# Optimization experiments

Hardware: AMD Instinct MI355X
Metric: run time of the kernel (lower is better)

## Reference

```python
import jax, jax.numpy as jnp
import numpy as np

B, N, D, Q, H = 8, 2048, 64, 16, 2
C = 2 * D + 1          # combined dim = 129
C8 = C // 8            # per-head qk dim = 16
K = 8192               # number of observed nodes
NEG = -9.0e15


def setup_inputs() -> dict:
    key = jax.random.key(0)
    ks = jax.random.split(key, 18)
    s = 0.05
    inp = {
        "x": jax.random.normal(ks[0], (B, N, D + 1), jnp.float32),
        "h": jax.random.normal(ks[1], (B, N, D), jnp.float32),
        "query_vectors": jax.random.normal(ks[2], (K, Q), jnp.float32),
        "adj": jax.random.randint(ks[3], (B, N, N), 0, 2, jnp.int32),
        "nodes_flat": jnp.arange(K, dtype=jnp.int32),
        # per-head attention projections (jax convention: x @ W + b)
        "Wq": jax.random.normal(ks[4], (H, C, C8), jnp.float32) * s,
        "bq": jax.random.normal(ks[5], (H, C8), jnp.float32) * s,
        "Wk": jax.random.normal(ks[6], (H, C, C8), jnp.float32) * s,
        "bk": jax.random.normal(ks[7], (H, C8), jnp.float32) * s,
        "Wv": jax.random.normal(ks[8], (H, C, C), jnp.float32) * s,
        "bv": jax.random.normal(ks[9], (H, C), jnp.float32) * s,
        # hypernetwork MLP_Param weights for reset / update / candidate gates
        "W_r": jax.random.normal(ks[10], (Q, C, D), jnp.float32) * s,
        "b_r": jax.random.normal(ks[11], (Q, D), jnp.float32) * s,
        "W_u": jax.random.normal(ks[12], (Q, C, D), jnp.float32) * s,
        "b_u": jax.random.normal(ks[13], (Q, D), jnp.float32) * s,
        "W_c": jax.random.normal(ks[14], (Q, C, D), jnp.float32) * s,
        "b_c": jax.random.normal(ks[15], (Q, D), jnp.float32) * s,
    }
    return inp


def _gate(x_sel, qv, W, b):
    # MLP_Param: W_n = einsum('nd,dio->nio', qv, W); out = x @ W_n + qv @ b
    # contract the combined dim first to avoid the [K, C, D] intermediate
    t = jnp.einsum('kc,qco->kqo', x_sel, W)      # [K, Q, D]
    return jnp.einsum('kq,kqo->ko', qv, t) + qv @ b


def reference(x, h, query_vectors, adj, nodes_flat,
              Wq, bq, Wk, bk, Wv, bv,
              W_r, b_r, W_u, b_u, W_c, b_c):
    combined = jnp.concatenate([x, h], axis=-1)                 # [B, N, C]
    q = jnp.einsum('bnc,hcd->hbnd', combined, Wq) + bq[:, None, None, :]
    k = jnp.einsum('bnc,hcd->hbnd', combined, Wk) + bk[:, None, None, :]
    v = jnp.einsum('bnc,hcd->hbnd', combined, Wv) + bv[:, None, None, :]
    scores = jnp.einsum('hbnd,hbmd->hbnm', q, k) / jnp.sqrt(jnp.float32(C8))
    scores = jax.nn.leaky_relu(scores, 0.2)
    scores = jnp.where(adj[None] == 0, NEG, scores)
    attn = jax.nn.softmax(scores, axis=-1)                      # [H, B, N, N]
    h_prime = jnp.einsum('hbnm,hbmc->hbnc', attn, v)
    comb_attn = h_prime.mean(axis=0)                            # [B, N, C]

    sel = comb_attn.reshape(-1, C)[nodes_flat]                  # [K, C]
    r = jax.nn.sigmoid(_gate(sel, query_vectors, W_r, b_r))     # [K, D]
    u = jax.nn.sigmoid(_gate(sel, query_vectors, W_u, b_u))     # [K, D]

    h_flat = h.reshape(-1, D)
    h_sel = r * h_flat[nodes_flat]                              # r * h[nodes_ind]
    h_flat = h_flat.at[nodes_flat].set(h_sel)
    h_new = h_flat.reshape(h.shape)

    comb_new = jnp.concatenate([x, h_new], axis=-1)             # [B, N, C]
    sel2 = comb_new.reshape(-1, C)[nodes_flat]
    cand = jnp.tanh(_gate(sel2, query_vectors, W_c, b_c))       # [K, D]

    return (1.0 - u) * h_sel + u * cand                         # [K, D]
```

## Files before the change

### kernel.cpp

```cpp
#include <hip/hip_runtime.h>
#include <hip/hip_bf16.h>


typedef _Float16 h2_t __attribute__((ext_vector_type(2)));
typedef _Float16 h8_t __attribute__((ext_vector_type(8)));
typedef float    f4_t __attribute__((ext_vector_type(4)));
#define MFMA16x32(a,b,c) __builtin_amdgcn_mfma_f32_16x16x32_f16(a,b,c,0,0,0)

#define OB_QG    0
#define OB_KG    524288
#define OB_VT    1048576
#define OB_MASK  5767168
#define OB_WALL  7864320
#define OB_HACC  7971840
#define OB_LSUM  16622592
#define OB_UBUF  16688128
#define OB_HSEL  18785280

__global__ __launch_bounds__(256) void pack_adj(const int* __restrict__ adj,
                                                unsigned* __restrict__ mask) {
    long tg = (long)blockIdx.x * 256 + threadIdx.x;
    for (int it = 0; it < 32; ++it) {
        long i = tg + (long)it * 524288;
        int a = adj[i];
        unsigned long long bal = __ballot(a != 0);
        if ((threadIdx.x & 63) == 0)
            *(unsigned long long*)(mask + (i >> 5)) = bal;
    }
}

__global__ __launch_bounds__(256) void repack_wall(
    const float* __restrict__ Wq, const float* __restrict__ bq,
    const float* __restrict__ Wk, const float* __restrict__ bk,
    const float* __restrict__ Wv, const float* __restrict__ bv,
    _Float16* __restrict__ Wall) {
    int idx = blockIdx.x * 256 + threadIdx.x;
    if (idx >= 6720) return;
    int ct = idx / 320;
    int rem = idx % 320;
    int s = rem >> 6, lane = rem & 63;
    int n = ct * 16 + (lane & 15);
    int quad = lane >> 4;
    int h2 = (n >= 164) ? 1 : 0;
    int nn = n - h2 * 164;
    h8_t v;
    #pragma unroll
    for (int j = 0; j < 8; ++j) {
        int k = s * 32 + quad * 8 + j;
        float f = 0.f;
        if (n < 328) {
            if (nn < 16) {
                if (k < 129)       f = Wq[(h2 * 129 + k) * 16 + nn];
                else if (k == 129) f = bq[h2 * 16 + nn];
            } else if (nn < 32) {
                int d = nn - 16;
                if (k < 129)       f = Wk[(h2 * 129 + k) * 16 + d];
                else if (k == 129) f = bk[h2 * 16 + d];
            } else {
                int vc = nn - 32;
                if (vc < 129) {
                    if (k < 129)       f = Wv[(h2 * 129 + k) * 129 + vc];
                    else if (k == 129) f = bv[h2 * 129 + vc];
                }
            }
        }
        v[j] = (_Float16)f;
    }
    *(h8_t*)(Wall + (size_t)idx * 8) = v;
}

__global__ __launch_bounds__(256) void repack_gates(
    const float* __restrict__ Wr, const float* __restrict__ br,
    const float* __restrict__ Wu, const float* __restrict__ bu,
    const float* __restrict__ Wc, const float* __restrict__ bc,
    _Float16* __restrict__ WtRu, _Float16* __restrict__ WtC) {
    int idx = blockIdx.x * 256 + threadIdx.x;
    if (idx < 35328) {
        int s = idx / 512;
        int rem = idx % 512;
        int ct = rem >> 6, lane = rem & 63;
        int o = ct * 16 + (lane & 15);
        int quad = lane >> 4;
        const float* W = (o < 64) ? Wr : Wu;
        const float* bb = (o < 64) ? br : bu;
        int oc = o & 63;
        h8_t v;
        #pragma unroll
        for (int j = 0; j < 8; ++j) {
            int kk = s * 32 + quad * 8 + j;
            float f = 0.f;
            if (kk < 2176) {
                int q = kk / 136, c = kk % 136;
                if (c < 129) f = W[(q * 129 + c) * 64 + oc];
            } else if (kk < 2192) {
                f = bb[(kk - 2176) * 64 + oc];
            }
            v[j] = (_Float16)f;
        }
        *(h8_t*)(WtRu + (size_t)idx * 8) = v;
    } else if (idx < 52992) {
        int i2 = idx - 35328;
        int s = i2 / 256;
        int rem = i2 % 256;
        int ct = rem >> 6, lane = rem & 63;
        int o = ct * 16 + (lane & 15);
        int quad = lane >> 4;
        h8_t v;
        #pragma unroll
        for (int j = 0; j < 8; ++j) {
            int kk = s * 32 + quad * 8 + j;
            float f = 0.f;
            if (kk < 2176) {
                int q = kk / 136, c = kk % 136;
                if (c < 129) f = Wc[(q * 129 + c) * 64 + o];
            } else if (kk < 2192) {
                f = bc[(kk - 2176) * 64 + o];
            }
            v[j] = (_Float16)f;
        }
        *(h8_t*)(WtC + (size_t)i2 * 8) = v;
    }
}

__global__ __launch_bounds__(256) void qkv_mfma(
    const float* __restrict__ x, const float* __restrict__ h,
    const _Float16* __restrict__ Wall,
    _Float16* __restrict__ qg, _Float16* __restrict__ kg,
    _Float16* __restrict__ vT) {
    __shared__ _Float16 at[16 * 168];
    int t = threadIdx.x;
    int row0 = blockIdx.x * 16;
    for (int idx = t; idx < 16 * 160; idx += 256) {
        int r = idx / 160, c = idx % 160;
        int grow = row0 + r;
        float v = 0.f;
        if (c < 65)       v = x[grow * 65 + c];
        else if (c < 129) v = h[grow * 64 + (c - 65)];
        else if (c == 129) v = 1.0f;
        at[r * 168 + c] = (_Float16)v;
    }
    __syncthreads();
    int lane = t & 63, w = t >> 6;
    int l16 = lane & 15, quad = lane >> 4;
    for (int ct = w; ct < 21; ct += 4) {
        f4_t acc; acc[0]=0.f; acc[1]=0.f; acc[2]=0.f; acc[3]=0.f;
        int n = ct * 16 + l16;
        const _Float16* wp = Wall + ((size_t)ct * 320 + lane) * 8;
        #pragma unroll
        for (int s = 0; s < 5; ++s) {
            h8_t a = *(const h8_t*)(at + l16 * 168 + s * 32 + quad * 8);
            h8_t b = *(const h8_t*)(wp + (size_t)s * 512);
            acc = MFMA16x32(a, b, acc);
        }
        if (n < 328) {
            int h2 = (n >= 164) ? 1 : 0;
            int nn = n - h2 * 164;
            #pragma unroll
            for (int r = 0; r < 4; ++r) {
                int grow = row0 + quad * 4 + r;
                _Float16 v = (_Float16)acc[r];
                if (nn < 16)      qg[(h2 * 8192 + grow) * 16 + nn] = v;
                else if (nn < 32) kg[(h2 * 8192 + grow) * 16 + (nn - 16)] = v;
                else              vT[((size_t)(h2 * 144 + (nn - 32))) * 8192 + grow] = v;
            }
        }
    }
}

__global__ __launch_bounds__(256) void attn_fused(
    const _Float16* __restrict__ qg, const _Float16* __restrict__ kg,
    const _Float16* __restrict__ vT, const unsigned* __restrict__ mask,
    float* __restrict__ hacc, float* __restrict__ lsum, int tps) {
    __shared__ _Float16 vsm[144 * 88];
    __shared__ _Float16 pT[4 * 16 * 88];
    int t = threadIdx.x;
    int nt = blockIdx.x, hb = blockIdx.y, sp = blockIdx.z;
    int h2 = hb >> 2, b = hb & 3;
    int base = h2 * 8192 + b * 2048;
    int n0 = nt * 64;
    int lane = t & 63, w = t >> 6;
    int l16 = lane & 15, q = lane >> 4;
    int qrow = n0 + w * 16 + l16;
    _Float16* pTw = pT + w * 16 * 88;
    h8_t zero8;
    #pragma unroll
    for (int i = 0; i < 8; ++i) zero8[i] = (_Float16)0.f;
    h8_t qf = zero8;
    if (q < 2) qf = *(const h8_t*)(qg + (base + qrow) * 16 + 8 * q);
    const unsigned* mrw = mask + (b * 2048 + qrow) * 64;
    f4_t acc[9];
    #pragma unroll
    for (int i = 0; i < 9; ++i) { acc[i][0]=0.f; acc[i][1]=0.f; acc[i][2]=0.f; acc[i][3]=0.f; }
    float l_run = 0.f;
    for (int mt = sp * tps; mt < sp * tps + tps; ++mt) {
        int m0 = mt * 64;
        __syncthreads();
        for (int idx = t; idx < 1152; idx += 256) {
            int c = idx >> 3, ch = idx & 7;
            *(uint4*)(vsm + c * 88 + ch * 8) =
                *(const uint4*)(vT + ((size_t)h2 * 144 + c) * 8192 + b * 2048 + m0 + ch * 8);
        }
        __syncthreads();
        uint2 mw = *(const uint2*)(mrw + (m0 >> 5));
        f4_t st[4];
        #pragma unroll
        for (int ct = 0; ct < 4; ++ct) {
            h8_t kf = zero8;
            if (q < 2)
                kf = *(const h8_t*)(kg + (base + m0 + 16 * ct + l16) * 16 + 8 * q);
            f4_t z4; z4[0]=0.f; z4[1]=0.f; z4[2]=0.f; z4[3]=0.f;
            st[ct] = MFMA16x32(kf, qf, z4);
        }
        #pragma unroll
        for (int ct = 0; ct < 4; ++ct) {
            unsigned wb = (ct < 2) ? mw.x : mw.y;
            float p[4];
            #pragma unroll
            for (int r = 0; r < 4; ++r) {
                float sc = st[ct][r] * 0.25f;
                sc = sc > 0.f ? sc : 0.2f * sc;
                int bit = ((ct & 1) ? 16 : 0) + 4 * q + r;
                p[r] = ((wb >> bit) & 1u) ? __expf(sc) : 0.f;
                l_run += p[r];
            }
            h2_t p01; p01[0] = (_Float16)p[0]; p01[1] = (_Float16)p[1];
            h2_t p23; p23[0] = (_Float16)p[2]; p23[1] = (_Float16)p[3];
            *(h2_t*)(pTw + l16 * 88 + 16 * ct + 4 * q)     = p01;
            *(h2_t*)(pTw + l16 * 88 + 16 * ct + 4 * q + 2) = p23;
        }
        #pragma unroll
        for (int kh = 0; kh < 2; ++kh) {
            h8_t ap = *(const h8_t*)(pTw + l16 * 88 + 32 * kh + 8 * q);
            #pragma unroll
            for (int nb = 0; nb < 9; ++nb) {
                h8_t vf = *(const h8_t*)(vsm + (16 * nb + l16) * 88 + 32 * kh + 8 * q);
                acc[nb] = MFMA16x32(ap, vf, acc[nb]);
            }
        }
    }
    l_run += __shfl_xor(l_run, 16);
    l_run += __shfl_xor(l_run, 32);
    float* hc = hacc + (size_t)h2 * 8192 * 132;
    if (q == 0)
        atomicAdd(lsum + h2 * 8192 + b * 2048 + n0 + w * 16 + l16, l_run);
    #pragma unroll
    for (int nb = 0; nb < 9; ++nb) {
        int vc = 16 * nb + l16;
        if (vc < 132) {
            #pragma unroll
            for (int r = 0; r < 4; ++r) {
                int grow = b * 2048 + n0 + w * 16 + 4 * q + r;
                atomicAdd(hc + grow * 132 + vc, acc[nb][r]);
            }
        }
    }
}

__global__ __launch_bounds__(256) void gate_ru_mfma(
    const float* __restrict__ hacc, const float* __restrict__ lsum,
    const int* __restrict__ nodes,
    const float* __restrict__ qv, const _Float16* __restrict__ WtRu,
    const float* __restrict__ hbuf,
    float* __restrict__ ubuf, float* __restrict__ hsel) {
    __shared__ _Float16 selh[16 * 152];
    __shared__ float qvs[16 * 17];
    __shared__ float invl[32];
    int t = threadIdx.x;
    int k0 = blockIdx.x * 16;
    if (t < 32) {
        int r = t >> 1, hh = t & 1;
        int grow = nodes[k0 + r];
        invl[t] = 0.5f / lsum[hh * 8192 + grow];
    }
    __syncthreads();
    for (int idx = t; idx < 16 * 136; idx += 256) {
        int r = idx / 136, c = idx % 136;
        _Float16 v = (_Float16)0.f;
        if (c < 132) {
            int grow = nodes[k0 + r];
            v = (_Float16)(hacc[grow * 132 + c] * invl[r * 2] +
                           hacc[8192 * 132 + grow * 132 + c] * invl[r * 2 + 1]);
        }
        selh[r * 152 + c] = v;
    }
    if (t < 256) {
        int r = t >> 4, q = t & 15;
        qvs[r * 17 + q] = qv[(k0 + r) * 16 + q];
    }
    __syncthreads();
    int lane = t & 63, w = t >> 6;
    int l16 = lane & 15, quad = lane >> 4;
    f4_t acc0, acc1;
    acc0[0]=0.f;acc0[1]=0.f;acc0[2]=0.f;acc0[3]=0.f;
    acc1[0]=0.f;acc1[1]=0.f;acc1[2]=0.f;acc1[3]=0.f;
    const _Float16* wp0 = WtRu + ((size_t)(2 * w) * 64 + lane) * 8;
    const _Float16* wp1 = wp0 + 512;
    for (int step = 0; step < 69; ++step) {
        h8_t a;
        if (step < 68) {
            int chunk = 4 * step + quad;
            int q = chunk / 17;
            int c0 = (chunk - q * 17) * 8;
            h8_t s8 = *(const h8_t*)(selh + l16 * 152 + c0);
            _Float16 qh = (_Float16)qvs[l16 * 17 + q];
            #pragma unroll
            for (int j = 0; j < 8; ++j) a[j] = s8[j] * qh;
        } else {
            int kl = quad * 8;
            #pragma unroll
            for (int j = 0; j < 8; ++j) {
                int kq = kl + j;
                a[j] = (kq < 16) ? (_Float16)qvs[l16 * 17 + kq] : (_Float16)0.f;
            }
        }
        h8_t b0 = *(const h8_t*)(wp0 + (size_t)step * 4096);
        h8_t b1 = *(const h8_t*)(wp1 + (size_t)step * 4096);
        acc0 = MFMA16x32(a, b0, acc0);
        acc1 = MFMA16x32(a, b1, acc1);
    }
    #pragma unroll
    for (int tt = 0; tt < 2; ++tt) {
        f4_t ac = tt ? acc1 : acc0;
        int o = (2 * w + tt) * 16 + l16;
        #pragma unroll
        for (int r = 0; r < 4; ++r) {
            int k = k0 + quad * 4 + r;
            float sg = 1.f / (1.f + __expf(-ac[r]));
            if (o < 64) {
                int grow = nodes[k];
                hsel[k * 64 + o] = sg * hbuf[grow * 64 + o];
            } else {
                ubuf[k * 64 + (o - 64)] = sg;
            }
        }
    }
}

__global__ __launch_bounds__(256) void gate_c_mfma(
    const float* __restrict__ x, const int* __restrict__ nodes,
    const float* __restrict__ qv, const _Float16* __restrict__ WtC,
    const float* __restrict__ hsel, const float* __restrict__ ubuf,
    float* __restrict__ out) {
    __shared__ _Float16 selh[16 * 152];
    __shared__ float qvs[16 * 17];
    int t = threadIdx.x;
    int k0 = blockIdx.x * 16;
    for (int idx = t; idx < 16 * 136; idx += 256) {
        int r = idx / 136, c = idx % 136;
        int k = k0 + r;
        _Float16 v = (_Float16)0.f;
        if (c < 65) {
            int grow = nodes[k];
            v = (_Float16)x[grow * 65 + c];
        } else if (c < 129) {
            v = (_Float16)hsel[k * 64 + (c - 65)];
        }
        selh[r * 152 + c] = v;
    }
    if (t < 256) {
        int r = t >> 4, q = t & 15;
        qvs[r * 17 + q] = qv[(k0 + r) * 16 + q];
    }
    __syncthreads();
    int lane = t & 63, w = t >> 6;
    int l16 = lane & 15, quad = lane >> 4;
    f4_t acc;
    acc[0]=0.f;acc[1]=0.f;acc[2]=0.f;acc[3]=0.f;
    const _Float16* wp = WtC + ((size_t)w * 64 + lane) * 8;
    for (int step = 0; step < 69; ++step) {
        h8_t a;
        if (step < 68) {
            int chunk = 4 * step + quad;
            int q = chunk / 17;
            int c0 = (chunk - q * 17) * 8;
            h8_t s8 = *(const h8_t*)(selh + l16 * 152 + c0);
            _Float16 qh = (_Float16)qvs[l16 * 17 + q];
            #pragma unroll
            for (int j = 0; j < 8; ++j) a[j] = s8[j] * qh;
        } else {
            int kl = quad * 8;
            #pragma unroll
            for (int j = 0; j < 8; ++j) {
                int kq = kl + j;
                a[j] = (kq < 16) ? (_Float16)qvs[l16 * 17 + kq] : (_Float16)0.f;
            }
        }
        h8_t b = *(const h8_t*)(wp + (size_t)step * 2048);
        acc = MFMA16x32(a, b, acc);
    }
    int o = w * 16 + l16;
    #pragma unroll
    for (int r = 0; r < 4; ++r) {
        int k = k0 + quad * 4 + r;
        float cv = tanhf(acc[r]);
        float hs = hsel[k * 64 + o];
        float uv = ubuf[k * 64 + o];
        out[k * 64 + o] = (1.f - uv) * hs + uv * cv;
    }
}

extern "C" void kernel_launch(void* const* d_in, const int* in_sizes, int n_in,
                              void* d_out, int out_size, void* d_ws, size_t ws_size,
                              hipStream_t stream) {
    const float* x   = (const float*)d_in[0];
    const float* h   = (const float*)d_in[1];
    const float* qv  = (const float*)d_in[2];
    const int*   adj = (const int*)d_in[3];
    const int*   nod = (const int*)d_in[4];
    const float* Wq  = (const float*)d_in[5];
    const float* bq  = (const float*)d_in[6];
    const float* Wk  = (const float*)d_in[7];
    const float* bk  = (const float*)d_in[8];
    const float* Wv  = (const float*)d_in[9];
    const float* bv  = (const float*)d_in[10];
    const float* Wr  = (const float*)d_in[11];
    const float* br  = (const float*)d_in[12];
    const float* Wu  = (const float*)d_in[13];
    const float* bu  = (const float*)d_in[14];
    const float* Wc  = (const float*)d_in[15];
    const float* bc  = (const float*)d_in[16];

    char* wsb = (char*)d_ws;
    _Float16* qg   = (_Float16*)(wsb + OB_QG);
    _Float16* kg   = (_Float16*)(wsb + OB_KG);
    _Float16* vT   = (_Float16*)(wsb + OB_VT);
    unsigned* mask = (unsigned*)(wsb + OB_MASK);
    _Float16* Wall = (_Float16*)(wsb + OB_WALL);
    float* hacc    = (float*)(wsb + OB_HACC);
    float* lsum    = (float*)(wsb + OB_LSUM);
    float* ubuf    = (float*)(wsb + OB_UBUF);
    float* hse     = (float*)(wsb + OB_HSEL);
    _Float16* WtRu = vT;
    _Float16* WtC  = vT + 69 * 8 * 64 * 8;

    pack_adj<<<dim3(2048), 256, 0, stream>>>(adj, mask);
    repack_wall<<<dim3(27), 256, 0, stream>>>(Wq, bq, Wk, bk, Wv, bv, Wall);
    qkv_mfma<<<dim3(512), 256, 0, stream>>>(x, h, Wall, qg, kg, vT);
    hipMemsetAsync(hacc, 0, (size_t)8650752 + 65536, stream);
    attn_fused<<<dim3(32, 8, 4), 256, 0, stream>>>(qg, kg, vT, mask,
                                                   hacc, lsum, 8);
    repack_gates<<<dim3(207), 256, 0, stream>>>(Wr, br, Wu, bu, Wc, bc,
                                                WtRu, WtC);
    gate_ru_mfma<<<dim3(512), 256, 0, stream>>>(hacc, lsum, nod, qv,
                                                WtRu, h, ubuf, hse);
    gate_c_mfma<<<dim3(512), 256, 0, stream>>>(x, nod, qv, WtC, hse, ubuf,
                                               (float*)d_out);
}
```

Baseline: 359.0 us.

## Fuse gate kernels, merge weight repacks, and coalesce vT stores via LDS

Merges the two weight-repack kernels into one launch, with the gate weights moved to their own workspace region instead of aliasing vT. Fuses the r/u gate and candidate gate kernels so the h_sel and u values stay in shared memory rather than making a round trip through global buffers. In qkv_mfma, the transposed V values are staged in LDS and written out as 16-byte vector stores instead of scattered 2-byte stores. In exchange, the fused gate kernel uses more shared memory per block and there is one fewer launch to overlap with.

```diff
diff --git a/kernel.cpp b/kernel.cpp
--- a/kernel.cpp
+++ b/kernel.cpp
@@ -14,8 +14,8 @@
 #define OB_WALL  7864320
 #define OB_HACC  7971840
 #define OB_LSUM  16622592
-#define OB_UBUF  16688128
-#define OB_HSEL  18785280
+#define OB_WTRU  16688128
+#define OB_WTC   17253376
 
 __global__ __launch_bounds__(256) void pack_adj(const int* __restrict__ adj,
                                                 unsigned* __restrict__ mask) {
@@ -29,55 +29,52 @@
     }
 }
 
-__global__ __launch_bounds__(256) void repack_wall(
+__global__ __launch_bounds__(256) void repack_all(
     const float* __restrict__ Wq, const float* __restrict__ bq,
     const float* __restrict__ Wk, const float* __restrict__ bk,
     const float* __restrict__ Wv, const float* __restrict__ bv,
-    _Float16* __restrict__ Wall) {
-    int idx = blockIdx.x * 256 + threadIdx.x;
-    if (idx >= 6720) return;
-    int ct = idx / 320;
-    int rem = idx % 320;
-    int s = rem >> 6, lane = rem & 63;
-    int n = ct * 16 + (lane & 15);
-    int quad = lane >> 4;
-    int h2 = (n >= 164) ? 1 : 0;
-    int nn = n - h2 * 164;
-    h8_t v;
-    #pragma unroll
-    for (int j = 0; j < 8; ++j) {
-        int k = s * 32 + quad * 8 + j;
-        float f = 0.f;
-        if (n < 328) {
-            if (nn < 16) {
-                if (k < 129)       f = Wq[(h2 * 129 + k) * 16 + nn];
-                else if (k == 129) f = bq[h2 * 16 + nn];
-            } else if (nn < 32) {
-                int d = nn - 16;
-                if (k < 129)       f = Wk[(h2 * 129 + k) * 16 + d];
-                else if (k == 129) f = bk[h2 * 16 + d];
-            } else {
-                int vc = nn - 32;
-                if (vc < 129) {
-                    if (k < 129)       f = Wv[(h2 * 129 + k) * 129 + vc];
-                    else if (k == 129) f = bv[h2 * 129 + vc];
-                }
-            }
-        }
-        v[j] = (_Float16)f;
-    }
-    *(h8_t*)(Wall + (size_t)idx * 8) = v;
-}
-
-__global__ __launch_bounds__(256) void repack_gates(
     const float* __restrict__ Wr, const float* __restrict__ br,
     const float* __restrict__ Wu, const float* __restrict__ bu,
     const float* __restrict__ Wc, const float* __restrict__ bc,
-    _Float16* __restrict__ WtRu, _Float16* __restrict__ WtC) {
+    _Float16* __restrict__ Wall, _Float16* __restrict__ WtRu,
+    _Float16* __restrict__ WtC) {
     int idx = blockIdx.x * 256 + threadIdx.x;
-    if (idx < 35328) {
-        int s = idx / 512;
-        int rem = idx % 512;
+    if (idx < 6720) {
+        int ct = idx / 320;
+        int rem = idx % 320;
+        int s = rem >> 6, lane = rem & 63;
+        int n = ct * 16 + (lane & 15);
+        int quad = lane >> 4;
+        int h2 = (n >= 164) ? 1 : 0;
+        int nn = n - h2 * 164;
+        h8_t v;
+        #pragma unroll
+        for (int j = 0; j < 8; ++j) {
+            int k = s * 32 + quad * 8 + j;
+            float f = 0.f;
+            if (n < 328) {
+                if (nn < 16) {
+                    if (k < 129)       f = Wq[(h2 * 129 + k) * 16 + nn];
+                    else if (k == 129) f = bq[h2 * 16 + nn];
+                } else if (nn < 32) {
+                    int d = nn - 16;
+                    if (k < 129)       f = Wk[(h2 * 129 + k) * 16 + d];
+                    else if (k == 129) f = bk[h2 * 16 + d];
+                } else {
+                    int vc = nn - 32;
+                    if (vc < 129) {
+                        if (k < 129)       f = Wv[(h2 * 129 + k) * 129 + vc];
+                        else if (k == 129) f = bv[h2 * 129 + vc];
+                    }
+                }
+            }
+            v[j] = (_Float16)f;
+        }
+        *(h8_t*)(Wall + (size_t)idx * 8) = v;
+    } else if (idx < 6720 + 35328) {
+        int i2 = idx - 6720;
+        int s = i2 / 512;
+        int rem = i2 % 512;
         int ct = rem >> 6, lane = rem & 63;
         int o = ct * 16 + (lane & 15);
         int quad = lane >> 4;
@@ -97,9 +94,9 @@
             }
             v[j] = (_Float16)f;
         }
-        *(h8_t*)(WtRu + (size_t)idx * 8) = v;
-    } else if (idx < 52992) {
-        int i2 = idx - 35328;
+        *(h8_t*)(WtRu + (size_t)i2 * 8) = v;
+    } else if (idx < 59712) {
+        int i2 = idx - 6720 - 35328;
         int s = i2 / 256;
         int rem = i2 % 256;
         int ct = rem >> 6, lane = rem & 63;
@@ -128,6 +125,7 @@
     _Float16* __restrict__ qg, _Float16* __restrict__ kg,
     _Float16* __restrict__ vT) {
     __shared__ _Float16 at[16 * 168];
+    __shared__ _Float16 vls[264 * 16];
     int t = threadIdx.x;
     int row0 = blockIdx.x * 16;
     for (int idx = t; idx < 16 * 160; idx += 256) {
@@ -157,13 +155,21 @@
             int nn = n - h2 * 164;
             #pragma unroll
             for (int r = 0; r < 4; ++r) {
-                int grow = row0 + quad * 4 + r;
+                int row = quad * 4 + r;
                 _Float16 v = (_Float16)acc[r];
-                if (nn < 16)      qg[(h2 * 8192 + grow) * 16 + nn] = v;
-                else if (nn < 32) kg[(h2 * 8192 + grow) * 16 + (nn - 16)] = v;
-                else              vT[((size_t)(h2 * 144 + (nn - 32))) * 8192 + grow] = v;
-            }
-        }
+                if (nn < 16)      qg[(h2 * 8192 + row0 + row) * 16 + nn] = v;
+                else if (nn < 32) kg[(h2 * 8192 + row0 + row) * 16 + (nn - 16)] = v;
+                else              vls[(h2 * 132 + (nn - 32)) * 16 + row] = v;
+            }
+        }
+    }
+    __syncthreads();
+    for (int idx = t; idx < 528; idx += 256) {
+        int col = idx >> 1, half = idx & 1;
+        int h2 = (col >= 132) ? 1 : 0;
+        int cc = col - h2 * 132;
+        uint4 v = ((const uint4*)vls)[idx];
+        *(uint4*)(vT + ((size_t)(h2 * 144 + cc)) * 8192 + row0 + half * 8) = v;
     }
 }
 
@@ -256,15 +262,18 @@
     }
 }
 
-__global__ __launch_bounds__(256) void gate_ru_mfma(
+__global__ __launch_bounds__(256) void gate_fused(
     const float* __restrict__ hacc, const float* __restrict__ lsum,
-    const int* __restrict__ nodes,
-    const float* __restrict__ qv, const _Float16* __restrict__ WtRu,
-    const float* __restrict__ hbuf,
-    float* __restrict__ ubuf, float* __restrict__ hsel) {
+    const int* __restrict__ nodes, const float* __restrict__ qv,
+    const _Float16* __restrict__ WtRu, const _Float16* __restrict__ WtC,
+    const float* __restrict__ hbuf, const float* __restrict__ x,
+    float* __restrict__ out) {
     __shared__ _Float16 selh[16 * 152];
+    __shared__ _Float16 selh2[16 * 152];
     __shared__ float qvs[16 * 17];
     __shared__ float invl[32];
+    __shared__ float hslds[16 * 66];
+    __shared__ float ulds[16 * 66];
     int t = threadIdx.x;
     int k0 = blockIdx.x * 16;
     if (t < 32) {
@@ -282,6 +291,12 @@
                            hacc[8192 * 132 + grow * 132 + c] * invl[r * 2 + 1]);
         }
         selh[r * 152 + c] = v;
+    }
+    for (int idx = t; idx < 16 * 136; idx += 256) {
+        int r = idx / 136, c = idx % 136;
+        _Float16 v = (_Float16)0.f;
+        if (c < 65) v = (_Float16)x[nodes[k0 + r] * 65 + c];
+        selh2[r * 152 + c] = v;
     }
     if (t < 256) {
         int r = t >> 4, q = t & 15;
@@ -324,48 +339,24 @@
         int o = (2 * w + tt) * 16 + l16;
         #pragma unroll
         for (int r = 0; r < 4; ++r) {
-            int k = k0 + quad * 4 + r;
+            int row = quad * 4 + r;
             float sg = 1.f / (1.f + __expf(-ac[r]));
             if (o < 64) {
-                int grow = nodes[k];
-                hsel[k * 64 + o] = sg * hbuf[grow * 64 + o];
+                float hs = sg * hbuf[nodes[k0 + row] * 64 + o];
+                hslds[row * 66 + o] = hs;
+                selh2[row * 152 + 65 + o] = (_Float16)hs;
             } else {
-                ubuf[k * 64 + (o - 64)] = sg;
-            }
-        }
-    }
-}
-
-__global__ __launch_bounds__(256) void gate_c_mfma(
-    const float* __restrict__ x, const int* __restrict__ nodes,
-    const float* __restrict__ qv, const _Float16* __restrict__ WtC,
-    const float* __restrict__ hsel, const float* __restrict__ ubuf,
-    float* __restrict__ out) {
-    __shared__ _Float16 selh[16 * 152];
-    __shared__ float qvs[16 * 17];
-    int t = threadIdx.x;
-    int k0 = blockIdx.x * 16;
-    for (int idx = t; idx < 16 * 136; idx += 256) {
-        int r = idx / 136, c = idx % 136;
-        int k = k0 + r;
-        _Float16 v = (_Float16)0.f;
-        if (c < 65) {
-            int grow = nodes[k];
-            v = (_Float16)x[grow * 65 + c];
-        } else if (c < 129) {
-            v = (_Float16)hsel[k * 64 + (c - 65)];
-        }
-        selh[r * 152 + c] = v;
-    }
-    if (t < 256) {
-        int r = t >> 4, q = t & 15;
-        qvs[r * 17 + q] = qv[(k0 + r) * 16 + q];
+                ulds[row * 66 + (o - 64)] = sg;
+            }
+        }
+    }
+    if (t < 112) {
+        int r = t / 7, c = 129 + (t % 7);
+        selh2[r * 152 + c] = (_Float16)0.f;
     }
     __syncthreads();
-    int lane = t & 63, w = t >> 6;
-    int l16 = lane & 15, quad = lane >> 4;
-    f4_t acc;
-    acc[0]=0.f;acc[1]=0.f;acc[2]=0.f;acc[3]=0.f;
+    f4_t acc2;
+    acc2[0]=0.f;acc2[1]=0.f;acc2[2]=0.f;acc2[3]=0.f;
     const _Float16* wp = WtC + ((size_t)w * 64 + lane) * 8;
     for (int step = 0; step < 69; ++step) {
         h8_t a;
@@ -373,7 +364,7 @@
             int chunk = 4 * step + quad;
             int q = chunk / 17;
             int c0 = (chunk - q * 17) * 8;
-            h8_t s8 = *(const h8_t*)(selh + l16 * 152 + c0);
+            h8_t s8 = *(const h8_t*)(selh2 + l16 * 152 + c0);
             _Float16 qh = (_Float16)qvs[l16 * 17 + q];
             #pragma unroll
             for (int j = 0; j < 8; ++j) a[j] = s8[j] * qh;
@@ -386,16 +377,16 @@
             }
         }
         h8_t b = *(const h8_t*)(wp + (size_t)step * 2048);
-        acc = MFMA16x32(a, b, acc);
+        acc2 = MFMA16x32(a, b, acc2);
     }
     int o = w * 16 + l16;
     #pragma unroll
     for (int r = 0; r < 4; ++r) {
-        int k = k0 + quad * 4 + r;
-        float cv = tanhf(acc[r]);
-        float hs = hsel[k * 64 + o];
-        float uv = ubuf[k * 64 + o];
-        out[k * 64 + o] = (1.f - uv) * hs + uv * cv;
+        int row = quad * 4 + r;
+        float cv = tanhf(acc2[r]);
+        float hs = hslds[row * 66 + o];
+        float uv = ulds[row * 66 + o];
+        out[(k0 + row) * 64 + o] = (1.f - uv) * hs + uv * cv;
     }
 }
 
@@ -428,21 +419,18 @@
     _Float16* Wall = (_Float16*)(wsb + OB_WALL);
     float* hacc    = (float*)(wsb + OB_HACC);
     float* lsum    = (float*)(wsb + OB_LSUM);
-    float* ubuf    = (float*)(wsb + OB_UBUF);
-    float* hse     = (float*)(wsb + OB_HSEL);
-    _Float16* WtRu = vT;
-    _Float16* WtC  = vT + 69 * 8 * 64 * 8;
+    _Float16* WtRu = (_Float16*)(wsb + OB_WTRU);
+    _Float16* WtC  = (_Float16*)(wsb + OB_WTC);
 
     pack_adj<<<dim3(2048), 256, 0, stream>>>(adj, mask);
-    repack_wall<<<dim3(27), 256, 0, stream>>>(Wq, bq, Wk, bk, Wv, bv, Wall);
+    repack_all<<<dim3(234), 256, 0, stream>>>(Wq, bq, Wk, bk, Wv, bv,
+                                              Wr, br, Wu, bu, Wc, bc,
+                                              Wall, WtRu, WtC);
     qkv_mfma<<<dim3(512), 256, 0, stream>>>(x, h, Wall, qg, kg, vT);
     hipMemsetAsync(hacc, 0, (size_t)8650752 + 65536, stream);
     attn_fused<<<dim3(32, 8, 4), 256, 0, stream>>>(qg, kg, vT, mask,
                                                    hacc, lsum, 8);
-    repack_gates<<<dim3(207), 256, 0, stream>>>(Wr, br, Wu, bu, Wc, bc,
-                                                WtRu, WtC);
-    gate_ru_mfma<<<dim3(512), 256, 0, stream>>>(hacc, lsum, nod, qv,
-                                                WtRu, h, ubuf, hse);
-    gate_c_mfma<<<dim3(512), 256, 0, stream>>>(x, nod, qv, WtC, hse, ubuf,
-                                               (float*)d_out);
-}
+    gate_fused<<<dim3(512), 256, 0, stream>>>(hacc, lsum, nod, qv,
+                                              WtRu, WtC, h, x,
+                                              (float*)d_out);
+}
```

Result: faster. 346.6 us (-3.5%).
